# Optimization experiments

Measured on AMD Instinct MI355X. Metric: run time of the kernel, lower is better.

## Reference

```python
import jax, jax.numpy as jnp
import numpy as np

B, S, D, E, F, K = 2, 4096, 1024, 8, 2048, 2


def setup_inputs() -> dict:
    key = jax.random.key(0)
    k1, k2, k3, k4 = jax.random.split(key, 4)
    return {
        "inputs_raw": jax.random.normal(k1, (B, S, D), dtype=jnp.float32),
        "gate_w": jax.random.normal(k2, (D, E), dtype=jnp.float32) * (D ** -0.5),
        "w1": jax.random.normal(k3, (E, D, F), dtype=jnp.float32) * (D ** -0.5),
        "w2": jax.random.normal(k4, (E, F, D), dtype=jnp.float32) * (F ** -0.5),
        "top_k": K,
    }


def reference(inputs_raw, gate_w, w1, w2, top_k):
    ishape = inputs_raw.shape
    x = inputs_raw.reshape(-1, ishape[-1])                 # [T, D]
    n_experts = gate_w.shape[-1]

    # --- gating: top-k logits, softmax over the selected k (float32, like the torch code) ---
    logits = x @ gate_w                                    # [T, E]
    top_vals, top_idx = jax.lax.top_k(logits, top_k)       # [T, K]
    top_w = jax.nn.softmax(top_vals.astype(jnp.float32), axis=-1).astype(x.dtype)
    # dense combine weights [T, E]; zero for unselected experts
    combine = jnp.einsum("tk,tke->te", top_w,
                         jax.nn.one_hot(top_idx, n_experts, dtype=x.dtype))

    # --- experts: D -> F (SiLU) -> D, evaluated densely and combined with gate weights ---
    h = jax.nn.silu(jnp.einsum("td,edf->etf", x, w1))      # [E, T, F]
    y = jnp.einsum("etf,efd->etd", h, w2)                  # [E, T, D]
    out = jnp.einsum("te,etd->td", combine, y)             # [T, D]
    return out.reshape(ishape)
```

## Files before the change

### kernel.cpp

```cpp
#include <hip/hip_runtime.h>
#include <cstdint>
#include <cstddef>

#define T_TOK 8192
#define DIM   1024
#define NE    8
#define FF    2048
#define TOPK  2

typedef __bf16 bf16x8 __attribute__((ext_vector_type(8)));
typedef float  floatx4 __attribute__((ext_vector_type(4)));

__device__ __forceinline__ unsigned short f2bf(float f) {
  unsigned int u = __float_as_uint(f);
  unsigned int r = 0x7FFFu + ((u >> 16) & 1u);
  return (unsigned short)((u + r) >> 16);
}

__device__ __forceinline__ void gl_lds16(const void* g, void* l) {
  __builtin_amdgcn_global_load_lds(
      (__attribute__((address_space(1))) void*)g,
      (__attribute__((address_space(3))) void*)l,
      16, 0, 0);
}

__global__ __launch_bounds__(256) void transpose_bf16_kernel(
    const float* __restrict__ in, unsigned short* __restrict__ out,
    int R, int C)
{
  __shared__ float tile[32][33];
  int e  = blockIdx.z;
  int c0 = blockIdx.x * 32, r0 = blockIdx.y * 32;
  int tx = threadIdx.x & 31, ty = threadIdx.x >> 5;
  const float* inp = in + (size_t)e * R * C;
  unsigned short* op = out + (size_t)e * R * C;
  for (int i = 0; i < 4; ++i)
    tile[ty + i * 8][tx] = inp[(size_t)(r0 + ty + i * 8) * C + c0 + tx];
  __syncthreads();
  for (int i = 0; i < 4; ++i)
    op[(size_t)(c0 + ty + i * 8) * R + r0 + tx] = f2bf(tile[tx][ty + i * 8]);
}

__global__ __launch_bounds__(256) void gate_kernel(
    const float* __restrict__ x, const float* __restrict__ gw,
    unsigned short* __restrict__ xb, int* __restrict__ tokExp,
    float* __restrict__ tokW, int* __restrict__ cnt)
{
  __shared__ float gwT[NE][DIM];
  int tid = threadIdx.x;
  if (blockIdx.x == 0 && tid < NE) cnt[tid] = 0;
  for (int i = tid; i < DIM * NE; i += 256) {
    int d = i >> 3, e = i & 7;
    gwT[e][d] = gw[i];
  }
  __syncthreads();

  int wv = tid >> 6, lane = tid & 63;
  int t = blockIdx.x * 4 + wv;
  const float* xrow = x + (size_t)t * DIM;
  unsigned short* xbrow = xb + (size_t)t * DIM;

  double acc[NE];
  for (int e = 0; e < NE; ++e) acc[e] = 0.0;

  for (int j = 0; j < 4; ++j) {
    float4 xv = ((const float4*)xrow)[j * 64 + lane];
    ushort4 s;
    s.x = f2bf(xv.x); s.y = f2bf(xv.y); s.z = f2bf(xv.z); s.w = f2bf(xv.w);
    ((ushort4*)xbrow)[j * 64 + lane] = s;
    double xd0 = (double)xv.x, xd1 = (double)xv.y;
    double xd2 = (double)xv.z, xd3 = (double)xv.w;
    for (int e = 0; e < NE; ++e) {
      float4 g = ((const float4*)&gwT[e][0])[j * 64 + lane];
      acc[e] += xd0 * (double)g.x + xd1 * (double)g.y +
                xd2 * (double)g.z + xd3 * (double)g.w;
    }
  }

  for (int s = 32; s > 0; s >>= 1)
    for (int e = 0; e < NE; ++e)
      acc[e] += __shfl_down(acc[e], s, 64);

  if (lane == 0) {
    int e0 = 0; double v0 = acc[0];
    for (int e = 1; e < NE; ++e) if (acc[e] > v0) { v0 = acc[e]; e0 = e; }
    int e1 = -1; double v1 = -1.0e300;
    for (int e = 0; e < NE; ++e) {
      if (e == e0) continue;
      if (acc[e] > v1) { v1 = acc[e]; e1 = e; }
    }
    float a = (float)v0, b = (float)v1;
    float eb = __expf(b - a);
    float den = 1.0f + eb;
    tokExp[t] = e0 | (e1 << 8);
    tokW[2 * t + 0] = 1.0f / den;
    tokW[2 * t + 1] = eb / den;
  }
}

__global__ __launch_bounds__(256) void assign_kernel(
    const int* __restrict__ tokExp, int* __restrict__ tokEnc,
    int* __restrict__ tIdx, int* __restrict__ cnt)
{
  int t = blockIdx.x * 256 + threadIdx.x;
  int lane = threadIdx.x & 63;
  unsigned long long below = (1ull << lane) - 1ull;
  int enc = tokExp[t];
  int e0 = enc & 0xFF, e1 = (enc >> 8) & 0xFF;
  int s0 = 0, s1 = 0;
  for (int e = 0; e < NE; ++e) {
    unsigned long long m0 = __ballot(e0 == e);
    unsigned long long m1 = __ballot(e1 == e);
    int c0 = __popcll(m0), c1 = __popcll(m1);
    int base = 0;
    if (lane == 0 && (c0 + c1) > 0)
      base = atomicAdd(&cnt[e], c0 + c1);
    base = __shfl(base, 0, 64);
    if (e0 == e) s0 = base + __popcll(m0 & below);
    if (e1 == e) s1 = base + c0 + __popcll(m1 & below);
  }
  tokEnc[2 * t + 0] = (e0 << 16) | s0;
  tokEnc[2 * t + 1] = (e1 << 16) | s1;
  tIdx[e0 * T_TOK + s0] = t;
  tIdx[e1 * T_TOK + s1] = t;
}

template<int KDIM>
__device__ __forceinline__ void mfma_core(
    const unsigned short* (&agp)[4], const unsigned short* (&bgp)[4],
    unsigned short* smem, floatx4 (&acc)[8][4])
{
  constexpr int NKT = KDIM / 64;
  const int tid = threadIdx.x, lane = tid & 63, w = tid >> 6;
  const int wm = w >> 2, wn = w & 3;
  const int quad = lane >> 4, li = lane & 15;

  unsigned short (*As)[8][256][8] = (unsigned short (*)[8][256][8])smem;
  unsigned short (*Bs)[8][256][8] = (unsigned short (*)[8][256][8])(smem + 32768);

  #define STAGE_A(BUF, KT, HALF) do { \
    gl_lds16(agp[(HALF)*2+0] + (KT)*64 + w*8, &As[BUF][w][(HALF)*128 +  0][0]); \
    gl_lds16(agp[(HALF)*2+1] + (KT)*64 + w*8, &As[BUF][w][(HALF)*128 + 64][0]); } while(0)
  #define STAGE_B(BUF, KT, HALF) do { \
    gl_lds16(bgp[(HALF)*2+0] + (KT)*64 + w*8, &Bs[BUF][w][(HALF)*128 +  0][0]); \
    gl_lds16(bgp[(HALF)*2+1] + (KT)*64 + w*8, &Bs[BUF][w][(HALF)*128 + 64][0]); } while(0)

  STAGE_B(0, 0, 0); STAGE_B(0, 0, 1);
  STAGE_A(0, 0, 0); STAGE_A(0, 0, 1);
  STAGE_B(1, 1, 0); STAGE_B(1, 1, 1);

  for (int t0 = 0; t0 < NKT; t0 += 2) {
    bf16x8 bf[4][2];
    #pragma unroll
    for (int q = 0; q < 4; ++q) {
      if (q == 0) STAGE_A(1, t0 + 1, 0);
      if (q == 1) { STAGE_A(1, t0 + 1, 1); if (t0 + 2 < NKT) STAGE_B(0, t0 + 2, 0); }
      if (q == 2) { if (t0 + 2 < NKT) STAGE_B(0, t0 + 2, 1); }
      if (q == 0) asm volatile("s_waitcnt vmcnt(6)" ::: "memory");
      asm volatile("s_barrier" ::: "memory");
      if (q == 0) {
        #pragma unroll
        for (int ni = 0; ni < 4; ++ni)
          #pragma unroll
          for (int kk = 0; kk < 2; ++kk)
            bf[ni][kk] = *(const bf16x8*)&Bs[0][kk * 4 + quad][wn * 64 + ni * 16 + li][0];
      }
      bf16x8 af[2][2];
      #pragma unroll
      for (int j = 0; j < 2; ++j)
        #pragma unroll
        for (int kk = 0; kk < 2; ++kk)
          af[j][kk] = *(const bf16x8*)&As[0][kk * 4 + quad][wm * 128 + (2 * q + j) * 16 + li][0];
      __builtin_amdgcn_s_setprio(1);
      #pragma unroll
      for (int j = 0; j < 2; ++j)
        #pragma unroll
        for (int ni = 0; ni < 4; ++ni)
          #pragma unroll
          for (int kk = 0; kk < 2; ++kk)
            acc[2 * q + j][ni] = __builtin_amdgcn_mfma_f32_16x16x32_bf16(
                af[j][kk], bf[ni][kk], acc[2 * q + j][ni], 0, 0, 0);
      __builtin_amdgcn_s_setprio(0);
      asm volatile("s_barrier" ::: "memory");
    }
    #pragma unroll
    for (int q = 0; q < 4; ++q) {
      if (q == 0) { if (t0 + 2 < NKT) STAGE_A(0, t0 + 2, 0); }
      if (q == 1) { if (t0 + 2 < NKT) STAGE_A(0, t0 + 2, 1); }
      if (q == 2) { if (t0 + 3 < NKT) STAGE_B(1, t0 + 3, 0); }
      if (q == 3) { if (t0 + 3 < NKT) STAGE_B(1, t0 + 3, 1); }
      if (q == 0) {
        if (t0 + 2 < NKT) asm volatile("s_waitcnt vmcnt(6)" ::: "memory");
        else              asm volatile("s_waitcnt vmcnt(0)" ::: "memory");
      }
      asm volatile("s_barrier" ::: "memory");
      if (q == 0) {
        #pragma unroll
        for (int ni = 0; ni < 4; ++ni)
          #pragma unroll
          for (int kk = 0; kk < 2; ++kk)
            bf[ni][kk] = *(const bf16x8*)&Bs[1][kk * 4 + quad][wn * 64 + ni * 16 + li][0];
      }
      bf16x8 af[2][2];
      #pragma unroll
      for (int j = 0; j < 2; ++j)
        #pragma unroll
        for (int kk = 0; kk < 2; ++kk)
          af[j][kk] = *(const bf16x8*)&As[1][kk * 4 + quad][wm * 128 + (2 * q + j) * 16 + li][0];
      __builtin_amdgcn_s_setprio(1);
      #pragma unroll
      for (int j = 0; j < 2; ++j)
        #pragma unroll
        for (int ni = 0; ni < 4; ++ni)
          #pragma unroll
          for (int kk = 0; kk < 2; ++kk)
            acc[2 * q + j][ni] = __builtin_amdgcn_mfma_f32_16x16x32_bf16(
                af[j][kk], bf[ni][kk], acc[2 * q + j][ni], 0, 0, 0);
      __builtin_amdgcn_s_setprio(0);
      asm volatile("s_barrier" ::: "memory");
    }
  }
  #undef STAGE_A
  #undef STAGE_B
}

__global__ __launch_bounds__(512, 2) void gemm1_kernel(
    const unsigned short* __restrict__ xb,
    const unsigned short* __restrict__ w1t,
    unsigned short* __restrict__ h,
    const int* __restrict__ tIdx, const int* __restrict__ cnt)
{
  int g = blockIdx.x;
  int e = g & 7;
  int b = g >> 3;
  int m = b & 31;
  int n = b >> 5;
  int count = cnt[e];
  int r0 = m * 256;
  if (r0 >= count) return;
  int n0 = n * 256;

  __shared__ __align__(16) unsigned short smem[2 * 8 * 256 * 8 * 2];

  int tid = threadIdx.x, lane = tid & 63;
  const unsigned short* agp[4];
  const unsigned short* bgp[4];
  #pragma unroll
  for (int gq = 0; gq < 4; ++gq) {
    int r = r0 + gq * 64 + lane; if (r > count - 1) r = count - 1;
    agp[gq] = xb + (size_t)tIdx[e * T_TOK + r] * DIM;
    bgp[gq] = w1t + ((size_t)e * FF + (n0 + gq * 64 + lane)) * DIM;
  }

  floatx4 acc[8][4];
  #pragma unroll
  for (int mi = 0; mi < 8; ++mi)
    #pragma unroll
    for (int ni = 0; ni < 4; ++ni)
      #pragma unroll
      for (int qq = 0; qq < 4; ++qq) acc[mi][ni][qq] = 0.0f;

  mfma_core<DIM>(agp, bgp, smem, acc);

  size_t hb = 0;
  for (int i = 0; i < e; ++i) hb += cnt[i];
  int w = tid >> 6, wm = w >> 2, wn = w & 3, quad = lane >> 4, li = lane & 15;
  for (int mi = 0; mi < 8; ++mi) {
    int rowb = wm * 128 + mi * 16 + quad * 4;
    for (int rr = 0; rr < 4; ++rr) {
      int r = r0 + rowb + rr;
      if (r >= count) continue;
      unsigned short* hrow = h + (hb + r) * FF + n0 + wn * 64 + li;
      for (int ni = 0; ni < 4; ++ni) {
        float v = acc[mi][ni][rr];
        float s = v / (1.0f + __expf(-v));
        hrow[ni * 16] = f2bf(s);
      }
    }
  }
}

__global__ __launch_bounds__(512, 2) void gemm2_kernel(
    const unsigned short* __restrict__ h,
    const unsigned short* __restrict__ w2t,
    float* __restrict__ yv,
    const int* __restrict__ cnt)
{
  int g = blockIdx.x;
  int e = g & 7;
  int b = g >> 3;
  int m = b & 31;
  int n = b >> 5;
  int count = cnt[e];
  int r0 = m * 256;
  if (r0 >= count) return;
  int n0 = n * 256;

  __shared__ __align__(16) unsigned short smem[2 * 8 * 256 * 8 * 2];

  int tid = threadIdx.x, lane = tid & 63;
  size_t yb = 0;
  for (int i = 0; i < e; ++i) yb += cnt[i];

  const unsigned short* agp[4];
  const unsigned short* bgp[4];
  #pragma unroll
  for (int gq = 0; gq < 4; ++gq) {
    int r = r0 + gq * 64 + lane; if (r > count - 1) r = count - 1;
    agp[gq] = h + (yb + r) * FF;
    bgp[gq] = w2t + ((size_t)e * DIM + (n0 + gq * 64 + lane)) * FF;
  }

  floatx4 acc[8][4];
  #pragma unroll
  for (int mi = 0; mi < 8; ++mi)
    #pragma unroll
    for (int ni = 0; ni < 4; ++ni)
      #pragma unroll
      for (int qq = 0; qq < 4; ++qq) acc[mi][ni][qq] = 0.0f;

  mfma_core<FF>(agp, bgp, smem, acc);

  int w = tid >> 6, wm = w >> 2, wn = w & 3, quad = lane >> 4, li = lane & 15;
  for (int mi = 0; mi < 8; ++mi) {
    int rowb = wm * 128 + mi * 16 + quad * 4;
    for (int rr = 0; rr < 4; ++rr) {
      int r = r0 + rowb + rr;
      if (r >= count) continue;
      float* yrow = yv + (yb + r) * DIM + n0 + wn * 64 + li;
      for (int ni = 0; ni < 4; ++ni)
        yrow[ni * 16] = acc[mi][ni][rr];
    }
  }
}

__global__ __launch_bounds__(256) void combine_kernel(
    const float* __restrict__ yv, const int* __restrict__ tokEnc,
    const float* __restrict__ tokW, const int* __restrict__ cnt,
    float* __restrict__ out)
{
  int t = blockIdx.x;
  int i = threadIdx.x;
  int enc0 = tokEnc[2 * t + 0], enc1 = tokEnc[2 * t + 1];
  float w0 = tokW[2 * t + 0], w1 = tokW[2 * t + 1];
  int x0 = enc0 >> 16, x1 = enc1 >> 16;
  int off0 = 0, off1 = 0, a = 0;
  for (int e = 0; e < NE; ++e) {
    if (e == x0) off0 = a;
    if (e == x1) off1 = a;
    a += cnt[e];
  }
  size_t row0 = (size_t)off0 + (enc0 & 0xFFFF);
  size_t row1 = (size_t)off1 + (enc1 & 0xFFFF);
  float4 va = ((const float4*)(yv + row0 * DIM))[i];
  float4 vb = ((const float4*)(yv + row1 * DIM))[i];
  float4 o;
  o.x = w0 * va.x + w1 * vb.x;
  o.y = w0 * va.y + w1 * vb.y;
  o.z = w0 * va.z + w1 * vb.z;
  o.w = w0 * va.w + w1 * vb.w;
  ((float4*)(out + (size_t)t * DIM))[i] = o;
}

extern "C" void kernel_launch(void* const* d_in, const int* in_sizes, int n_in,
                              void* d_out, int out_size, void* d_ws, size_t ws_size,
                              hipStream_t stream)
{
  const float* x  = (const float*)d_in[0];
  const float* gw = (const float*)d_in[1];
  const float* w1 = (const float*)d_in[2];
  const float* w2 = (const float*)d_in[3];
  float* out = (float*)d_out;

  size_t o = 0;
  auto alloc = [&](size_t bytes) {
    void* p = (char*)d_ws + o;
    o += (bytes + 255) & ~(size_t)255;
    return p;
  };
  unsigned short* xb   = (unsigned short*)alloc((size_t)T_TOK * DIM * 2);
  unsigned short* w1t  = (unsigned short*)alloc((size_t)NE * DIM * FF * 2);
  unsigned short* w2t  = (unsigned short*)alloc((size_t)NE * DIM * FF * 2);
  unsigned short* hbuf = (unsigned short*)alloc((size_t)T_TOK * TOPK * FF * 2);
  float*          yv   = (float*)alloc((size_t)T_TOK * TOPK * DIM * 4);
  int*   tIdx   = (int*)alloc((size_t)NE * T_TOK * 4);
  int*   tokEnc = (int*)alloc((size_t)2 * T_TOK * 4);
  float* tokW   = (float*)alloc((size_t)2 * T_TOK * 4);
  int*   tokExp = (int*)alloc((size_t)T_TOK * 4);
  int*   cnt    = (int*)alloc((size_t)NE * 4);

  transpose_bf16_kernel<<<dim3(FF / 32, DIM / 32, NE), 256, 0, stream>>>(w1, w1t, DIM, FF);
  transpose_bf16_kernel<<<dim3(DIM / 32, FF / 32, NE), 256, 0, stream>>>(w2, w2t, FF, DIM);

  gate_kernel<<<T_TOK / 4, 256, 0, stream>>>(x, gw, xb, tokExp, tokW, cnt);
  assign_kernel<<<T_TOK / 256, 256, 0, stream>>>(tokExp, tokEnc, tIdx, cnt);

  gemm1_kernel<<<NE * 8 * 32, 512, 0, stream>>>(xb, w1t, hbuf, tIdx, cnt);
  gemm2_kernel<<<NE * 4 * 32, 512, 0, stream>>>(hbuf, w2t, yv, cnt);
  combine_kernel<<<T_TOK, 256, 0, stream>>>(yv, tokEnc, tokW, cnt, out);
}
```

Before: 620.1 us.

## Fuse weight transposes, reorder gemm1 grid, retile gemm2 to 128x128 blocks

Merges the two weight transpose launches into one kernel that uses 64x64 tiles, float4 loads, converts to bf16 before staging in LDS, and writes ushort4. Reorders the gemm1 block index so blocks sharing an expert and n-group are adjacent, aiming for better weight reuse in L2. Rewrites gemm2 to use 128x128 tiles with 256 threads and a simple single-buffered LDS loop, which gives more blocks and better occupancy. The cost is losing the pipelined mfma_core path in gemm2.

```diff
diff --git a/kernel.cpp b/kernel.cpp
--- a/kernel.cpp
+++ b/kernel.cpp
@@ -24,21 +24,40 @@
       16, 0, 0);
 }
 
-__global__ __launch_bounds__(256) void transpose_bf16_kernel(
-    const float* __restrict__ in, unsigned short* __restrict__ out,
-    int R, int C)
-{
-  __shared__ float tile[32][33];
-  int e  = blockIdx.z;
-  int c0 = blockIdx.x * 32, r0 = blockIdx.y * 32;
-  int tx = threadIdx.x & 31, ty = threadIdx.x >> 5;
-  const float* inp = in + (size_t)e * R * C;
-  unsigned short* op = out + (size_t)e * R * C;
-  for (int i = 0; i < 4; ++i)
-    tile[ty + i * 8][tx] = inp[(size_t)(r0 + ty + i * 8) * C + c0 + tx];
+__global__ __launch_bounds__(256) void transpose2_bf16_kernel(
+    const float* __restrict__ w1, unsigned short* __restrict__ w1t,
+    const float* __restrict__ w2, unsigned short* __restrict__ w2t)
+{
+  __shared__ unsigned short tile[64][68];
+  int z = blockIdx.z;
+  int e = z & 7, sel = z >> 3;
+  int R = sel ? FF : DIM;
+  int C = sel ? DIM : FF;
+  const float* inp = (sel ? w2 : w1) + (size_t)e * R * C;
+  unsigned short* op = (sel ? w2t : w1t) + (size_t)e * R * C;
+  int nc = C >> 6;
+  int bx = blockIdx.x;
+  int c0 = (bx % nc) * 64, r0 = (bx / nc) * 64;
+  int t4 = threadIdx.x & 15, ry = threadIdx.x >> 4;
+  #pragma unroll
+  for (int p = 0; p < 4; ++p) {
+    int r = ry + p * 16;
+    float4 v = *(const float4*)&inp[(size_t)(r0 + r) * C + c0 + t4 * 4];
+    ushort4 sv;
+    sv.x = f2bf(v.x); sv.y = f2bf(v.y); sv.z = f2bf(v.z); sv.w = f2bf(v.w);
+    *(ushort4*)&tile[r][t4 * 4] = sv;
+  }
   __syncthreads();
-  for (int i = 0; i < 4; ++i)
-    op[(size_t)(c0 + ty + i * 8) * R + r0 + tx] = f2bf(tile[tx][ty + i * 8]);
+  #pragma unroll
+  for (int p = 0; p < 4; ++p) {
+    int cy = ry + p * 16;
+    ushort4 s;
+    s.x = tile[t4 * 4 + 0][cy];
+    s.y = tile[t4 * 4 + 1][cy];
+    s.z = tile[t4 * 4 + 2][cy];
+    s.w = tile[t4 * 4 + 3][cy];
+    *(ushort4*)&op[(size_t)(c0 + cy) * R + r0 + t4 * 4] = s;
+  }
 }
 
 __global__ __launch_bounds__(256) void gate_kernel(
@@ -233,12 +252,13 @@
   int g = blockIdx.x;
   int e = g & 7;
   int b = g >> 3;
-  int m = b & 31;
-  int n = b >> 5;
+  int nl = b & 3;
+  int m = (b >> 2) & 31;
+  int phase = b >> 7;
   int count = cnt[e];
   int r0 = m * 256;
   if (r0 >= count) return;
-  int n0 = n * 256;
+  int n0 = (phase * 4 + nl) * 256;
 
   __shared__ __align__(16) unsigned short smem[2 * 8 * 256 * 8 * 2];
 
@@ -280,7 +300,7 @@
   }
 }
 
-__global__ __launch_bounds__(512, 2) void gemm2_kernel(
+__global__ __launch_bounds__(256, 4) void gemm2_kernel(
     const unsigned short* __restrict__ h,
     const unsigned short* __restrict__ w2t,
     float* __restrict__ yv,
@@ -289,45 +309,66 @@
   int g = blockIdx.x;
   int e = g & 7;
   int b = g >> 3;
-  int m = b & 31;
-  int n = b >> 5;
+  int phase = b >> 8;
+  int m = (b >> 2) & 63;
+  int nl = b & 3;
   int count = cnt[e];
-  int r0 = m * 256;
+  int r0 = m * 128;
   if (r0 >= count) return;
-  int n0 = n * 256;
-
-  __shared__ __align__(16) unsigned short smem[2 * 8 * 256 * 8 * 2];
-
-  int tid = threadIdx.x, lane = tid & 63;
+  int n0 = (phase * 4 + nl) * 128;
+
+  __shared__ __align__(16) unsigned short As[8][128][8];
+  __shared__ __align__(16) unsigned short Bs[8][128][8];
+
+  int tid = threadIdx.x, lane = tid & 63, w = tid >> 6;
+  int wr = w >> 1, wc = w & 1;
+  int quad = lane >> 4, li = lane & 15;
   size_t yb = 0;
   for (int i = 0; i < e; ++i) yb += cnt[i];
 
-  const unsigned short* agp[4];
-  const unsigned short* bgp[4];
-  #pragma unroll
-  for (int gq = 0; gq < 4; ++gq) {
-    int r = r0 + gq * 64 + lane; if (r > count - 1) r = count - 1;
-    agp[gq] = h + (yb + r) * FF;
-    bgp[gq] = w2t + ((size_t)e * DIM + (n0 + gq * 64 + lane)) * FF;
-  }
-
-  floatx4 acc[8][4];
-  #pragma unroll
-  for (int mi = 0; mi < 8; ++mi)
-    #pragma unroll
+  const unsigned short* ag[2];
+  const unsigned short* bg[2];
+  for (int c = 0; c < 2; ++c) {
+    int mm = c * 64 + lane;
+    int r = r0 + mm; if (r > count - 1) r = count - 1;
+    ag[c] = h + (yb + r) * FF;
+    bg[c] = w2t + ((size_t)e * DIM + (n0 + mm)) * FF;
+  }
+
+  floatx4 acc[4][4];
+  for (int mi = 0; mi < 4; ++mi)
     for (int ni = 0; ni < 4; ++ni)
-      #pragma unroll
-      for (int qq = 0; qq < 4; ++qq) acc[mi][ni][qq] = 0.0f;
-
-  mfma_core<FF>(agp, bgp, smem, acc);
-
-  int w = tid >> 6, wm = w >> 2, wn = w & 3, quad = lane >> 4, li = lane & 15;
-  for (int mi = 0; mi < 8; ++mi) {
-    int rowb = wm * 128 + mi * 16 + quad * 4;
+      for (int q = 0; q < 4; ++q) acc[mi][ni][q] = 0.0f;
+
+  for (int k0 = 0; k0 < FF; k0 += 64) {
+    __syncthreads();
+    for (int kk = 0; kk < 2; ++kk) {
+      int kq = w + kk * 4;
+      gl_lds16(ag[0] + k0 + kq * 8, &As[kq][0][0]);
+      gl_lds16(ag[1] + k0 + kq * 8, &As[kq][64][0]);
+      gl_lds16(bg[0] + k0 + kq * 8, &Bs[kq][0][0]);
+      gl_lds16(bg[1] + k0 + kq * 8, &Bs[kq][64][0]);
+    }
+    __syncthreads();
+    for (int ks = 0; ks < 2; ++ks) {
+      bf16x8 af[4], bf[4];
+      for (int mi = 0; mi < 4; ++mi)
+        af[mi] = *(const bf16x8*)&As[ks * 4 + quad][wr * 64 + mi * 16 + li][0];
+      for (int ni = 0; ni < 4; ++ni)
+        bf[ni] = *(const bf16x8*)&Bs[ks * 4 + quad][wc * 64 + ni * 16 + li][0];
+      for (int mi = 0; mi < 4; ++mi)
+        for (int ni = 0; ni < 4; ++ni)
+          acc[mi][ni] = __builtin_amdgcn_mfma_f32_16x16x32_bf16(
+              af[mi], bf[ni], acc[mi][ni], 0, 0, 0);
+    }
+  }
+
+  for (int mi = 0; mi < 4; ++mi) {
+    int rowb = wr * 64 + mi * 16 + quad * 4;
     for (int rr = 0; rr < 4; ++rr) {
       int r = r0 + rowb + rr;
       if (r >= count) continue;
-      float* yrow = yv + (yb + r) * DIM + n0 + wn * 64 + li;
+      float* yrow = yv + (yb + r) * DIM + n0 + wc * 64 + li;
       for (int ni = 0; ni < 4; ++ni)
         yrow[ni * 16] = acc[mi][ni][rr];
     }
@@ -389,13 +430,12 @@
   int*   tokExp = (int*)alloc((size_t)T_TOK * 4);
   int*   cnt    = (int*)alloc((size_t)NE * 4);
 
-  transpose_bf16_kernel<<<dim3(FF / 32, DIM / 32, NE), 256, 0, stream>>>(w1, w1t, DIM, FF);
-  transpose_bf16_kernel<<<dim3(DIM / 32, FF / 32, NE), 256, 0, stream>>>(w2, w2t, FF, DIM);
+  transpose2_bf16_kernel<<<dim3(512, 1, 2 * NE), 256, 0, stream>>>(w1, w1t, w2, w2t);
 
   gate_kernel<<<T_TOK / 4, 256, 0, stream>>>(x, gw, xb, tokExp, tokW, cnt);
   assign_kernel<<<T_TOK / 256, 256, 0, stream>>>(tokExp, tokEnc, tIdx, cnt);
 
-  gemm1_kernel<<<NE * 8 * 32, 512, 0, stream>>>(xb, w1t, hbuf, tIdx, cnt);
-  gemm2_kernel<<<NE * 4 * 32, 512, 0, stream>>>(hbuf, w2t, yv, cnt);
+  gemm1_kernel<<<NE * 2 * 32 * 4, 512, 0, stream>>>(xb, w1t, hbuf, tIdx, cnt);
+  gemm2_kernel<<<4096, 256, 0, stream>>>(hbuf, w2t, yv, cnt);
   combine_kernel<<<T_TOK, 256, 0, stream>>>(yv, tokEnc, tokW, cnt, out);
 }
```

Result: no change. 630.9 us (+1.7%).
